# Kernel optimization log

Hardware: AMD Instinct MI355X
Metric: run time of the kernel (lower is better)

The kernel has to match this reference:

```python
import jax, jax.numpy as jnp
import numpy as np

HID_X = 64
MLP_RATIO = 4
EPS_NORM = 1e-12  # F.normalize default eps
EPS_RMS = 1e-6


def _l2norm_dim2(w):
    # normalize along dim=-2 (the input-feature axis of each per-sample matrix)
    n = jnp.sqrt(jnp.sum(w * w, axis=-2, keepdims=True))
    return w / jnp.maximum(n, EPS_NORM)


def setup_inputs() -> dict:
    key = jax.random.key(0)
    k1, k2, k3, k4 = jax.random.split(key, 4)
    B, N, D, S = 64, 4096, HID_X, 1024
    total = 3 * D * D * MLP_RATIO
    x = jax.random.normal(k1, (B, N, D), dtype=jnp.float32)
    s = jax.random.normal(k2, (B, S), dtype=jnp.float32)
    W_pg = jax.random.normal(k3, (S, total), dtype=jnp.float32) * 0.02
    b_pg = jax.random.normal(k4, (total,), dtype=jnp.float32) * 0.01
    scale = jnp.ones((D,), dtype=jnp.float32)
    return {"x": x, "s": s, "W_pg": W_pg, "b_pg": b_pg, "scale": scale}


def reference(x, s, W_pg, b_pg, scale):
    B, N, D = x.shape
    H = D * MLP_RATIO
    # hypernetwork: generate per-sample MLP weights
    mlp_params = s @ W_pg + b_pg  # [B, 3*D*H]
    g_p, v_p, f_p = jnp.split(mlp_params, 3, axis=-1)
    fc1_gate = _l2norm_dim2(g_p.reshape(B, D, H))
    fc1_value = _l2norm_dim2(v_p.reshape(B, D, H))
    fc2 = _l2norm_dim2(f_p.reshape(B, H, D))
    # RMSNorm (eps=1e-6)
    rrms = jax.lax.rsqrt(jnp.mean(x * x, axis=-1, keepdims=True) + EPS_RMS)
    xn = x * rrms * scale
    gate = jnp.einsum('bnd,bdh->bnh', xn, fc1_gate)
    value = jnp.einsum('bnd,bdh->bnh', xn, fc1_value)
    h = jax.nn.silu(gate) * value
    out = jnp.einsum('bnh,bhd->bnd', h, fc2) + x
    return out
```

## Files before the change

kernel.cpp:

```cpp
#include <hip/hip_runtime.h>
#include <hip/hip_bf16.h>

#define BB 64
#define NN 4096
#define DD 64
#define HH 256
#define SS 1024
#define TOTAL 49152
#define MAT_ELEMS 16384

typedef __bf16 bf16x8 __attribute__((ext_vector_type(8)));
typedef float  f32x4  __attribute__((ext_vector_type(4)));

__global__ __launch_bounds__(256, 4) void k1_gemm(
    const float* __restrict__ s, const float* __restrict__ W,
    const float* __restrict__ bias, float* __restrict__ params)
{
    const int n0 = blockIdx.x * 64;
    const int t  = threadIdx.x;
    const int tx = t & 15, ty = t >> 4;

    __shared__ float sA[64 * 36];
    __shared__ float sB[32 * 68];

    float acc[4][4] = {};

    for (int k0 = 0; k0 < SS; k0 += 32) {
        #pragma unroll
        for (int i = 0; i < 2; i++) {
            int f4i = t + i * 256;
            int m = f4i >> 3, k4 = f4i & 7;
            float4 v = *(const float4*)&s[m * SS + k0 + k4 * 4];
            *(float4*)&sA[m * 36 + k4 * 4] = v;
        }
        #pragma unroll
        for (int i = 0; i < 2; i++) {
            int f4i = t + i * 256;
            int kk = f4i >> 4, n4 = f4i & 15;
            float4 v = *(const float4*)&W[(size_t)(k0 + kk) * TOTAL + n0 + n4 * 4];
            *(float4*)&sB[kk * 68 + n4 * 4] = v;
        }
        __syncthreads();
        #pragma unroll
        for (int kk = 0; kk < 32; kk++) {
            float4 b = *(const float4*)&sB[kk * 68 + tx * 4];
            float a0 = sA[(ty * 4 + 0) * 36 + kk];
            float a1 = sA[(ty * 4 + 1) * 36 + kk];
            float a2 = sA[(ty * 4 + 2) * 36 + kk];
            float a3 = sA[(ty * 4 + 3) * 36 + kk];
            acc[0][0] += a0 * b.x; acc[0][1] += a0 * b.y; acc[0][2] += a0 * b.z; acc[0][3] += a0 * b.w;
            acc[1][0] += a1 * b.x; acc[1][1] += a1 * b.y; acc[1][2] += a1 * b.z; acc[1][3] += a1 * b.w;
            acc[2][0] += a2 * b.x; acc[2][1] += a2 * b.y; acc[2][2] += a2 * b.z; acc[2][3] += a2 * b.w;
            acc[3][0] += a3 * b.x; acc[3][1] += a3 * b.y; acc[3][2] += a3 * b.z; acc[3][3] += a3 * b.w;
        }
        __syncthreads();
    }

    #pragma unroll
    for (int r = 0; r < 4; r++) {
        int m = ty * 4 + r;
        int n = n0 + tx * 4;
        float4 bv = *(const float4*)&bias[n];
        float4 o;
        o.x = acc[r][0] + bv.x; o.y = acc[r][1] + bv.y;
        o.z = acc[r][2] + bv.z; o.w = acc[r][3] + bv.w;
        *(float4*)&params[(size_t)m * TOTAL + n] = o;
    }
}

__global__ __launch_bounds__(256) void k2_fc1(
    const float* __restrict__ params, __bf16* __restrict__ WgT, __bf16* __restrict__ WvT)
{
    const int b   = blockIdx.x >> 1;
    const int mat = blockIdx.x & 1;
    const int t   = threadIdx.x;
    __shared__ float sh[64 * 257];
    __shared__ float rnorm[HH];

    const float* src = params + (size_t)b * TOTAL + mat * MAT_ELEMS;
    #pragma unroll
    for (int i = 0; i < 64; i++) {
        int idx = t + i * 256;
        int d = idx >> 8, h = idx & 255;
        sh[d * 257 + h] = src[idx];
    }
    __syncthreads();
    {
        float sum = 0.f;
        #pragma unroll
        for (int d = 0; d < 64; d++) {
            float v = sh[d * 257 + t];
            sum += v * v;
        }
        rnorm[t] = 1.0f / fmaxf(sqrtf(sum), 1e-12f);
    }
    __syncthreads();
    __bf16* dst = (mat ? WvT : WgT) + (size_t)b * MAT_ELEMS;
    #pragma unroll
    for (int i = 0; i < 64; i++) {
        int idx = t + i * 256;
        int h = idx >> 6, d = idx & 63;
        dst[idx] = (__bf16)(sh[d * 257 + h] * rnorm[h]);
    }
}

__global__ __launch_bounds__(256) void k2_fc2(
    const float* __restrict__ params, __bf16* __restrict__ WfT)
{
    const int b = blockIdx.x;
    const int t = threadIdx.x;
    __shared__ float sh[256 * 65];
    __shared__ float psum[4 * 64];
    __shared__ float rnorm[DD];

    const float* src = params + (size_t)b * TOTAL + 2 * MAT_ELEMS;
    #pragma unroll
    for (int i = 0; i < 64; i++) {
        int idx = t + i * 256;
        int h = idx >> 6, d = idx & 63;
        sh[h * 65 + d] = src[idx];
    }
    __syncthreads();
    {
        int d = t & 63, q = t >> 6;
        float sum = 0.f;
        #pragma unroll
        for (int i = 0; i < 64; i++) {
            int h = q * 64 + i;
            float v = sh[h * 65 + d];
            sum += v * v;
        }
        psum[q * 64 + d] = sum;
    }
    __syncthreads();
    if (t < 64) {
        float sum = psum[t] + psum[64 + t] + psum[128 + t] + psum[192 + t];
        rnorm[t] = 1.0f / fmaxf(sqrtf(sum), 1e-12f);
    }
    __syncthreads();
    __bf16* dst = WfT + (size_t)b * MAT_ELEMS;
    #pragma unroll
    for (int i = 0; i < 64; i++) {
        int idx = t + i * 256;
        int d = idx >> 8, h = idx & 255;
        dst[idx] = (__bf16)(sh[h * 65 + d] * rnorm[d]);
    }
}

__global__ __launch_bounds__(256, 2) void k3_fused(
    const float* __restrict__ x, const float* __restrict__ scale,
    const __bf16* __restrict__ WgT, const __bf16* __restrict__ WvT,
    const __bf16* __restrict__ WfT, float* __restrict__ out)
{
    const int b    = blockIdx.x >> 4;
    const int rb   = blockIdx.x & 15;
    const int t    = threadIdx.x;
    const int w    = t >> 6;
    const int lane = t & 63;
    const int l15  = lane & 15;
    const int quad = lane >> 4;

    __shared__ __bf16 xn_sh[256 * 72];
    __shared__ __bf16 h_sh[4 * 64 * 40];

    const size_t row_base = ((size_t)b * NN + rb * 256) * DD;

    const float scl = scale[lane];
    for (int r = 0; r < 64; r++) {
        int row = w * 64 + r;
        float v = x[row_base + (size_t)row * DD + lane];
        float ss = v * v;
        #pragma unroll
        for (int off = 32; off; off >>= 1) ss += __shfl_xor(ss, off, 64);
        float rr = rsqrtf(ss * (1.0f / 64.0f) + 1e-6f);
        xn_sh[row * 72 + lane] = (__bf16)(v * rr * scl);
    }

    bf16x8 afrag[4][2];
    #pragma unroll
    for (int mt = 0; mt < 4; mt++)
        #pragma unroll
        for (int ks = 0; ks < 2; ks++)
            afrag[mt][ks] = *(const bf16x8*)&xn_sh[(w * 64 + mt * 16 + l15) * 72 + ks * 32 + quad * 8];

    f32x4 oacc[4][4] = {};
    const __bf16* wg_b = WgT + (size_t)b * MAT_ELEMS;
    const __bf16* wv_b = WvT + (size_t)b * MAT_ELEMS;
    const __bf16* wf_b = WfT + (size_t)b * MAT_ELEMS;
    __bf16* hbuf = &h_sh[w * 64 * 40];

    for (int np = 0; np < 8; np++) {
        #pragma unroll
        for (int sub = 0; sub < 2; sub++) {
            int nt = np * 2 + sub;
            const __bf16* gp = &wg_b[(nt * 16 + l15) * 64 + quad * 8];
            const __bf16* vp = &wv_b[(nt * 16 + l15) * 64 + quad * 8];
            bf16x8 bg0 = *(const bf16x8*)(gp);
            bf16x8 bg1 = *(const bf16x8*)(gp + 32);
            bf16x8 bv0 = *(const bf16x8*)(vp);
            bf16x8 bv1 = *(const bf16x8*)(vp + 32);
            #pragma unroll
            for (int mt = 0; mt < 4; mt++) {
                f32x4 g = {0.f, 0.f, 0.f, 0.f}, vv = {0.f, 0.f, 0.f, 0.f};
                g  = __builtin_amdgcn_mfma_f32_16x16x32_bf16(afrag[mt][0], bg0, g, 0, 0, 0);
                g  = __builtin_amdgcn_mfma_f32_16x16x32_bf16(afrag[mt][1], bg1, g, 0, 0, 0);
                vv = __builtin_amdgcn_mfma_f32_16x16x32_bf16(afrag[mt][0], bv0, vv, 0, 0, 0);
                vv = __builtin_amdgcn_mfma_f32_16x16x32_bf16(afrag[mt][1], bv1, vv, 0, 0, 0);
                #pragma unroll
                for (int r = 0; r < 4; r++) {
                    float gv = g[r];
                    float hval = (gv / (1.0f + __expf(-gv))) * vv[r];
                    hbuf[(mt * 16 + quad * 4 + r) * 40 + sub * 16 + l15] = (__bf16)hval;
                }
            }
        }
        bf16x8 bff[4];
        #pragma unroll
        for (int dt = 0; dt < 4; dt++)
            bff[dt] = *(const bf16x8*)&wf_b[(dt * 16 + l15) * 256 + np * 32 + quad * 8];
        #pragma unroll
        for (int mt = 0; mt < 4; mt++) {
            bf16x8 ah = *(const bf16x8*)&hbuf[(mt * 16 + l15) * 40 + quad * 8];
            #pragma unroll
            for (int dt = 0; dt < 4; dt++)
                oacc[mt][dt] = __builtin_amdgcn_mfma_f32_16x16x32_bf16(ah, bff[dt], oacc[mt][dt], 0, 0, 0);
        }
    }

    #pragma unroll
    for (int mt = 0; mt < 4; mt++) {
        int r0 = w * 64 + mt * 16 + quad * 4;
        #pragma unroll
        for (int rg = 0; rg < 4; rg++) {
            size_t roff = row_base + (size_t)(r0 + rg) * DD;
            #pragma unroll
            for (int dt = 0; dt < 4; dt++) {
                int col = dt * 16 + l15;
                out[roff + col] = oacc[mt][dt][rg] + x[roff + col];
            }
        }
    }
}

extern "C" void kernel_launch(void* const* d_in, const int* in_sizes, int n_in,
                              void* d_out, int out_size, void* d_ws, size_t ws_size,
                              hipStream_t stream)
{
    const float* x     = (const float*)d_in[0];
    const float* s     = (const float*)d_in[1];
    const float* W_pg  = (const float*)d_in[2];
    const float* b_pg  = (const float*)d_in[3];
    const float* scale = (const float*)d_in[4];
    float* out = (float*)d_out;

    char* ws = (char*)d_ws;
    float*  params = (float*)ws;
    __bf16* WgT    = (__bf16*)(ws + 12582912);
    __bf16* WvT    = (__bf16*)(ws + 14680064);
    __bf16* WfT    = (__bf16*)(ws + 16777216);

    k1_gemm<<<TOTAL / 64, 256, 0, stream>>>(s, W_pg, b_pg, params);
    k2_fc1<<<BB * 2, 256, 0, stream>>>(params, WgT, WvT);
    k2_fc2<<<BB, 256, 0, stream>>>(params, WfT);
    k3_fused<<<BB * 16, 256, 0, stream>>>(x, scale, WgT, WvT, WfT, out);
}
```

Baseline: 466.8 us.

## Split normalize and fused MLP kernels into more blocks, compute RMSNorm in registers

The fc1/fc2 normalize kernels now split each matrix across 2 blocks, doubling the grid and shrinking shared memory per block. The fused MLP kernel handles 128 rows per block instead of 256 (2 m-tiles per wave), raises the occupancy hint to 4, and computes RMSNorm straight into MFMA A-fragments from vectorized global loads, dropping the xn shared-memory staging. All weight fragments for an iteration are loaded up front, and SiLU uses a hardware reciprocal instead of a divide. The aim is more parallelism and latency hiding, at the cost of loading each weight matrix twice as often per batch.

New measurement: 457.0 us. -2.1%, faster.

```diff
diff --git a/kernel.cpp b/kernel.cpp
--- a/kernel.cpp
+++ b/kernel.cpp
@@ -71,25 +71,26 @@
 __global__ __launch_bounds__(256) void k2_fc1(
     const float* __restrict__ params, __bf16* __restrict__ WgT, __bf16* __restrict__ WvT)
 {
-    const int b   = blockIdx.x >> 1;
-    const int mat = blockIdx.x & 1;
+    const int b   = blockIdx.x >> 2;
+    const int mat = (blockIdx.x >> 1) & 1;
+    const int hh  = blockIdx.x & 1;
     const int t   = threadIdx.x;
-    __shared__ float sh[64 * 257];
-    __shared__ float rnorm[HH];
-
-    const float* src = params + (size_t)b * TOTAL + mat * MAT_ELEMS;
-    #pragma unroll
-    for (int i = 0; i < 64; i++) {
-        int idx = t + i * 256;
-        int d = idx >> 8, h = idx & 255;
-        sh[d * 257 + h] = src[idx];
-    }
-    __syncthreads();
-    {
+    __shared__ float sh[64 * 130];
+    __shared__ float rnorm[128];
+
+    const float* src = params + (size_t)b * TOTAL + mat * MAT_ELEMS + hh * 128;
+    #pragma unroll
+    for (int i = 0; i < 32; i++) {
+        int idx = t + i * 256;
+        int d = idx >> 7, h = idx & 127;
+        sh[d * 130 + h] = src[d * 256 + h];
+    }
+    __syncthreads();
+    if (t < 128) {
         float sum = 0.f;
         #pragma unroll
         for (int d = 0; d < 64; d++) {
-            float v = sh[d * 257 + t];
+            float v = sh[d * 130 + t];
             sum += v * v;
         }
         rnorm[t] = 1.0f / fmaxf(sqrtf(sum), 1e-12f);
@@ -97,139 +98,156 @@
     __syncthreads();
     __bf16* dst = (mat ? WvT : WgT) + (size_t)b * MAT_ELEMS;
     #pragma unroll
-    for (int i = 0; i < 64; i++) {
-        int idx = t + i * 256;
-        int h = idx >> 6, d = idx & 63;
-        dst[idx] = (__bf16)(sh[d * 257 + h] * rnorm[h]);
+    for (int i = 0; i < 32; i++) {
+        int idx = t + i * 256;
+        int hl = idx >> 6, d = idx & 63;
+        dst[(hh * 128 + hl) * 64 + d] = (__bf16)(sh[d * 130 + hl] * rnorm[hl]);
     }
 }
 
 __global__ __launch_bounds__(256) void k2_fc2(
     const float* __restrict__ params, __bf16* __restrict__ WfT)
 {
-    const int b = blockIdx.x;
-    const int t = threadIdx.x;
-    __shared__ float sh[256 * 65];
-    __shared__ float psum[4 * 64];
-    __shared__ float rnorm[DD];
-
-    const float* src = params + (size_t)b * TOTAL + 2 * MAT_ELEMS;
-    #pragma unroll
-    for (int i = 0; i < 64; i++) {
-        int idx = t + i * 256;
-        int h = idx >> 6, d = idx & 63;
-        sh[h * 65 + d] = src[idx];
+    const int b  = blockIdx.x >> 1;
+    const int dh = blockIdx.x & 1;
+    const int t  = threadIdx.x;
+    __shared__ float sh[256 * 33];
+    __shared__ float psum[8 * 32];
+    __shared__ float rnorm[32];
+
+    const float* src = params + (size_t)b * TOTAL + 2 * MAT_ELEMS + dh * 32;
+    #pragma unroll
+    for (int i = 0; i < 32; i++) {
+        int idx = t + i * 256;
+        int h = idx >> 5, d = idx & 31;
+        sh[h * 33 + d] = src[h * 64 + d];
     }
     __syncthreads();
     {
-        int d = t & 63, q = t >> 6;
+        int d = t & 31, seg = t >> 5;
         float sum = 0.f;
         #pragma unroll
-        for (int i = 0; i < 64; i++) {
-            int h = q * 64 + i;
-            float v = sh[h * 65 + d];
+        for (int hi = 0; hi < 32; hi++) {
+            float v = sh[(seg * 32 + hi) * 33 + d];
             sum += v * v;
         }
-        psum[q * 64 + d] = sum;
-    }
-    __syncthreads();
-    if (t < 64) {
-        float sum = psum[t] + psum[64 + t] + psum[128 + t] + psum[192 + t];
+        psum[seg * 32 + d] = sum;
+    }
+    __syncthreads();
+    if (t < 32) {
+        float sum = 0.f;
+        #pragma unroll
+        for (int seg = 0; seg < 8; seg++) sum += psum[seg * 32 + t];
         rnorm[t] = 1.0f / fmaxf(sqrtf(sum), 1e-12f);
     }
     __syncthreads();
     __bf16* dst = WfT + (size_t)b * MAT_ELEMS;
     #pragma unroll
-    for (int i = 0; i < 64; i++) {
+    for (int i = 0; i < 32; i++) {
         int idx = t + i * 256;
         int d = idx >> 8, h = idx & 255;
-        dst[idx] = (__bf16)(sh[h * 65 + d] * rnorm[d]);
-    }
-}
-
-__global__ __launch_bounds__(256, 2) void k3_fused(
+        dst[(dh * 32 + d) * 256 + h] = (__bf16)(sh[h * 33 + d] * rnorm[d]);
+    }
+}
+
+__global__ __launch_bounds__(256, 4) void k3_fused(
     const float* __restrict__ x, const float* __restrict__ scale,
     const __bf16* __restrict__ WgT, const __bf16* __restrict__ WvT,
     const __bf16* __restrict__ WfT, float* __restrict__ out)
 {
-    const int b    = blockIdx.x >> 4;
-    const int rb   = blockIdx.x & 15;
+    const int b    = blockIdx.x >> 5;
+    const int rb   = blockIdx.x & 31;
     const int t    = threadIdx.x;
     const int w    = t >> 6;
     const int lane = t & 63;
     const int l15  = lane & 15;
     const int quad = lane >> 4;
 
-    __shared__ __bf16 xn_sh[256 * 72];
-    __shared__ __bf16 h_sh[4 * 64 * 40];
-
-    const size_t row_base = ((size_t)b * NN + rb * 256) * DD;
-
-    const float scl = scale[lane];
-    for (int r = 0; r < 64; r++) {
-        int row = w * 64 + r;
-        float v = x[row_base + (size_t)row * DD + lane];
-        float ss = v * v;
-        #pragma unroll
-        for (int off = 32; off; off >>= 1) ss += __shfl_xor(ss, off, 64);
+    __shared__ __bf16 h_sh[4 * 32 * 36];
+
+    const size_t row_base = ((size_t)b * NN + rb * 128) * DD;
+
+    float sc[16];
+    *(float4*)&sc[0]  = *(const float4*)&scale[quad * 8];
+    *(float4*)&sc[4]  = *(const float4*)&scale[quad * 8 + 4];
+    *(float4*)&sc[8]  = *(const float4*)&scale[32 + quad * 8];
+    *(float4*)&sc[12] = *(const float4*)&scale[32 + quad * 8 + 4];
+
+    bf16x8 afrag[2][2];
+    #pragma unroll
+    for (int mt = 0; mt < 2; mt++) {
+        int row = w * 32 + mt * 16 + l15;
+        const float* xp = &x[row_base + (size_t)row * DD + quad * 8];
+        float v[16];
+        *(float4*)&v[0]  = *(const float4*)(xp);
+        *(float4*)&v[4]  = *(const float4*)(xp + 4);
+        *(float4*)&v[8]  = *(const float4*)(xp + 32);
+        *(float4*)&v[12] = *(const float4*)(xp + 36);
+        float ss = 0.f;
+        #pragma unroll
+        for (int j = 0; j < 16; j++) ss += v[j] * v[j];
+        ss += __shfl_xor(ss, 16, 64);
+        ss += __shfl_xor(ss, 32, 64);
         float rr = rsqrtf(ss * (1.0f / 64.0f) + 1e-6f);
-        xn_sh[row * 72 + lane] = (__bf16)(v * rr * scl);
-    }
-
-    bf16x8 afrag[4][2];
-    #pragma unroll
-    for (int mt = 0; mt < 4; mt++)
-        #pragma unroll
-        for (int ks = 0; ks < 2; ks++)
-            afrag[mt][ks] = *(const bf16x8*)&xn_sh[(w * 64 + mt * 16 + l15) * 72 + ks * 32 + quad * 8];
-
-    f32x4 oacc[4][4] = {};
+        #pragma unroll
+        for (int j = 0; j < 8; j++) {
+            afrag[mt][0][j] = (__bf16)(v[j] * rr * sc[j]);
+            afrag[mt][1][j] = (__bf16)(v[8 + j] * rr * sc[8 + j]);
+        }
+    }
+
+    f32x4 oacc[2][4] = {};
     const __bf16* wg_b = WgT + (size_t)b * MAT_ELEMS;
     const __bf16* wv_b = WvT + (size_t)b * MAT_ELEMS;
     const __bf16* wf_b = WfT + (size_t)b * MAT_ELEMS;
-    __bf16* hbuf = &h_sh[w * 64 * 40];
+    __bf16* hbuf = &h_sh[w * 32 * 36];
 
     for (int np = 0; np < 8; np++) {
+        bf16x8 bg[2][2], bv[2][2], bf[4];
         #pragma unroll
         for (int sub = 0; sub < 2; sub++) {
             int nt = np * 2 + sub;
             const __bf16* gp = &wg_b[(nt * 16 + l15) * 64 + quad * 8];
             const __bf16* vp = &wv_b[(nt * 16 + l15) * 64 + quad * 8];
-            bf16x8 bg0 = *(const bf16x8*)(gp);
-            bf16x8 bg1 = *(const bf16x8*)(gp + 32);
-            bf16x8 bv0 = *(const bf16x8*)(vp);
-            bf16x8 bv1 = *(const bf16x8*)(vp + 32);
+            bg[sub][0] = *(const bf16x8*)(gp);
+            bg[sub][1] = *(const bf16x8*)(gp + 32);
+            bv[sub][0] = *(const bf16x8*)(vp);
+            bv[sub][1] = *(const bf16x8*)(vp + 32);
+        }
+        #pragma unroll
+        for (int dt = 0; dt < 4; dt++)
+            bf[dt] = *(const bf16x8*)&wf_b[(dt * 16 + l15) * 256 + np * 32 + quad * 8];
+
+        #pragma unroll
+        for (int sub = 0; sub < 2; sub++) {
             #pragma unroll
-            for (int mt = 0; mt < 4; mt++) {
+            for (int mt = 0; mt < 2; mt++) {
                 f32x4 g = {0.f, 0.f, 0.f, 0.f}, vv = {0.f, 0.f, 0.f, 0.f};
-                g  = __builtin_amdgcn_mfma_f32_16x16x32_bf16(afrag[mt][0], bg0, g, 0, 0, 0);
-                g  = __builtin_amdgcn_mfma_f32_16x16x32_bf16(afrag[mt][1], bg1, g, 0, 0, 0);
-                vv = __builtin_amdgcn_mfma_f32_16x16x32_bf16(afrag[mt][0], bv0, vv, 0, 0, 0);
-                vv = __builtin_amdgcn_mfma_f32_16x16x32_bf16(afrag[mt][1], bv1, vv, 0, 0, 0);
+                g  = __builtin_amdgcn_mfma_f32_16x16x32_bf16(afrag[mt][0], bg[sub][0], g, 0, 0, 0);
+                g  = __builtin_amdgcn_mfma_f32_16x16x32_bf16(afrag[mt][1], bg[sub][1], g, 0, 0, 0);
+                vv = __builtin_amdgcn_mfma_f32_16x16x32_bf16(afrag[mt][0], bv[sub][0], vv, 0, 0, 0);
+                vv = __builtin_amdgcn_mfma_f32_16x16x32_bf16(afrag[mt][1], bv[sub][1], vv, 0, 0, 0);
                 #pragma unroll
                 for (int r = 0; r < 4; r++) {
                     float gv = g[r];
-                    float hval = (gv / (1.0f + __expf(-gv))) * vv[r];
-                    hbuf[(mt * 16 + quad * 4 + r) * 40 + sub * 16 + l15] = (__bf16)hval;
+                    float sig = __builtin_amdgcn_rcpf(1.0f + __expf(-gv));
+                    float hval = gv * sig * vv[r];
+                    hbuf[(mt * 16 + quad * 4 + r) * 36 + sub * 16 + l15] = (__bf16)hval;
                 }
             }
         }
-        bf16x8 bff[4];
-        #pragma unroll
-        for (int dt = 0; dt < 4; dt++)
-            bff[dt] = *(const bf16x8*)&wf_b[(dt * 16 + l15) * 256 + np * 32 + quad * 8];
-        #pragma unroll
-        for (int mt = 0; mt < 4; mt++) {
-            bf16x8 ah = *(const bf16x8*)&hbuf[(mt * 16 + l15) * 40 + quad * 8];
+        #pragma unroll
+        for (int mt = 0; mt < 2; mt++) {
+            bf16x8 ah = *(const bf16x8*)&hbuf[(mt * 16 + l15) * 36 + quad * 8];
             #pragma unroll
             for (int dt = 0; dt < 4; dt++)
-                oacc[mt][dt] = __builtin_amdgcn_mfma_f32_16x16x32_bf16(ah, bff[dt], oacc[mt][dt], 0, 0, 0);
-        }
-    }
-
-    #pragma unroll
-    for (int mt = 0; mt < 4; mt++) {
-        int r0 = w * 64 + mt * 16 + quad * 4;
+                oacc[mt][dt] = __builtin_amdgcn_mfma_f32_16x16x32_bf16(ah, bf[dt], oacc[mt][dt], 0, 0, 0);
+        }
+    }
+
+    #pragma unroll
+    for (int mt = 0; mt < 2; mt++) {
+        int r0 = w * 32 + mt * 16 + quad * 4;
         #pragma unroll
         for (int rg = 0; rg < 4; rg++) {
             size_t roff = row_base + (size_t)(r0 + rg) * DD;
@@ -260,7 +278,7 @@
     __bf16* WfT    = (__bf16*)(ws + 16777216);
 
     k1_gemm<<<TOTAL / 64, 256, 0, stream>>>(s, W_pg, b_pg, params);
-    k2_fc1<<<BB * 2, 256, 0, stream>>>(params, WgT, WvT);
-    k2_fc2<<<BB, 256, 0, stream>>>(params, WfT);
-    k3_fused<<<BB * 16, 256, 0, stream>>>(x, scale, WgT, WvT, WfT, out);
-}
+    k2_fc1<<<BB * 4, 256, 0, stream>>>(params, WgT, WvT);
+    k2_fc2<<<BB * 2, 256, 0, stream>>>(params, WfT);
+    k3_fused<<<BB * 32, 256, 0, stream>>>(x, scale, WgT, WvT, WfT, out);
+}
```
